# Optimization experiments

Hardware: AMD Instinct MI355X
Metric: run time of the kernel (lower is better)

Reference implementation:

```python
import jax, jax.numpy as jnp
import numpy as np

NUM_ROUTING = 3

def squash(v, axis=-1):
    # scale = s2 / (1 + s2) / sqrt(s2), same as the TF source (no epsilon)
    s2 = jnp.sum(jnp.square(v), axis=axis, keepdims=True)
    scale = s2 / (1.0 + s2) / jnp.sqrt(s2)
    return scale * v


def setup_inputs() -> dict:
    key = jax.random.key(0)
    k1, k2 = jax.random.split(key)
    B, I, D = 128, 1152, 8   # batch, input_num_capsule, input_dim_vector
    C, E = 32, 16            # num_capsule, dim_vector
    x = jax.random.normal(k1, (B, I, D), dtype=jnp.float32)
    W = jax.random.normal(k2, (I, C, D, E), dtype=jnp.float32) * 0.05
    return {"x": x, "W": W}


def reference(x, W):
    # x: [B, I, D]; W: [I, C, D, E]
    B, I, D = x.shape
    C, E = W.shape[1], W.shape[3]
    # inputs_hat: u_hat[b,i,c,e] = sum_d x[b,i,d] * W[i,c,d,e]
    # (the TF code serializes this over batch via tf.scan; math is a batched GEMM)
    u_hat = jnp.einsum('bid,icde->bice', x, W)  # [B, I, C, E]
    # routing logits; TF bias has shape [1, I, C, 1, 1] and becomes per-batch
    # [B, I, C, 1, 1] after the first += (broadcast). We track [*, I, C].
    b = jnp.zeros((1, I, C), dtype=x.dtype)
    outputs = None
    for i in range(NUM_ROUTING):
        c = jax.nn.softmax(b, axis=2)[..., None]           # [*, I, C, 1]
        s = jnp.sum(c * u_hat, axis=1, keepdims=True)      # [B, 1, C, E]
        outputs = squash(s)                                # [B, 1, C, E]
        if i != NUM_ROUTING - 1:
            b = b + jnp.sum(u_hat * outputs, axis=-1)      # [B, I, C]
    return outputs.reshape(B, C, E)
```

## Files before the change

kernel.cpp:

```cpp
#include <hip/hip_runtime.h>
#include <hip/hip_fp16.h>
#include <math.h>

#define BATCH 128
#define NI    1152
#define ND    8
#define NC    32
#define NE    16
#define NROUT 3

#define ISPLIT     128
#define ICHUNK     (NI / ISPLIT)
#define BT         16
#define NB         4
#define RT_THREADS 256
#define CROW       68
#define TLDSW      (NC * CROW)
#define TILEF      (NC * ND * NE)
#define SQ_THREADS 256

typedef _Float16 h2 __attribute__((ext_vector_type(2)));
typedef unsigned int uint;

__device__ __forceinline__ h2 cvt_pk(float a, float b) {
    auto r = __builtin_amdgcn_cvt_pkrtz(a, b);
    union { decltype(r) i; h2 o; } u; u.i = r; return u.o;
}
__device__ __forceinline__ uint h2u(h2 v) { union { h2 h; uint u; } x; x.h = v; return x.u; }
__device__ __forceinline__ h2 u2h(uint v) { union { uint u; h2 h; } x; x.u = v; return x.h; }

#if __has_builtin(__builtin_amdgcn_fdot2)
#define FDOT2(a, b, c) __builtin_amdgcn_fdot2((a), (b), (c), false)
#else
__device__ __forceinline__ float FDOT2(h2 a, h2 b, float c) {
    return c + (float)a.x * (float)b.x + (float)a.y * (float)b.y;
}
#endif

template<int CTRL>
__device__ __forceinline__ float dpp_add(float v) {
    int t = __builtin_amdgcn_update_dpp(0, __float_as_int(v), CTRL, 0xF, 0xF, true);
    return v + __int_as_float(t);
}

__device__ __forceinline__ float xor32_sum(float v) {
#if __has_builtin(__builtin_amdgcn_permlane32_swap)
    auto r = __builtin_amdgcn_permlane32_swap(__float_as_int(v), __float_as_int(v), false, false);
    return __int_as_float(r[0]) + __int_as_float(r[1]);
#else
    return v + __shfl_xor(v, 32);
#endif
}
__device__ __forceinline__ float xor16_sum(float v) {
#if __has_builtin(__builtin_amdgcn_permlane16_swap)
    auto r = __builtin_amdgcn_permlane16_swap(__float_as_int(v), __float_as_int(v), false, false);
    return __int_as_float(r[0]) + __int_as_float(r[1]);
#else
    int s = __builtin_amdgcn_ds_swizzle(__float_as_int(v), 0x401F);
    return v + __int_as_float(s);
#endif
}

__device__ __forceinline__ float sum_over_e8(float v) {
    v = dpp_add<0xB1>(v);
    v = dpp_add<0x4E>(v);
    v = dpp_add<0x141>(v);
    return v;
}

__global__ __launch_bounds__(RT_THREADS)
void route_iter_kernel(const float* __restrict__ x, const float* __restrict__ W,
                       const float* __restrict__ o_sum, void* __restrict__ s_part,
                       int iter, int nslice, int use_atomic)
{
    __shared__ uint Wh[ICHUNK * TLDSW];

    const int tid = threadIdx.x;
    const int c   = tid & 31;
    const int eh  = (tid >> 5) & 1;
    int wid;
    asm("v_mov_b32 %0, %1" : "=v"(wid) : "v"(tid >> 6));
    const int ic  = blockIdx.x;
    const int bt  = blockIdx.y;
    const int i0  = ic * ICHUNK;
    const int b0  = bt * BT + wid * NB;
    const int e0  = eh * 8;

    {
        const float4* wsrc = (const float4*)(W + (size_t)i0 * TILEF);
        const int p0 = tid;
#pragma unroll
        for (int t = 0; t < ICHUNK; ++t) {
            float4 fa[2], fb[2];
#pragma unroll
            for (int r = 0; r < 2; ++r) {
                int p  = p0 + r * RT_THREADS;
                int cc = p >> 4, q = p & 15;
                int dp = q >> 2, e4 = q & 3;
                int base = t * 1024 + cc * 32 + dp * 8 + e4;
                fa[r] = wsrc[base];
                fb[r] = wsrc[base + 4];
            }
#pragma unroll
            for (int r = 0; r < 2; ++r) {
                int p  = p0 + r * RT_THREADS;
                int cc = p >> 4, q = p & 15;
                int dp = q >> 2, e4 = q & 3;
                uint* wb = &Wh[t * TLDSW + cc * CROW + e4 * 16 + dp];
                wb[0]  = h2u(cvt_pk(fa[r].x, fb[r].x));
                wb[4]  = h2u(cvt_pk(fa[r].y, fb[r].y));
                wb[8]  = h2u(cvt_pk(fa[r].z, fb[r].z));
                wb[12] = h2u(cvt_pk(fa[r].w, fb[r].w));
            }
        }
    }

    float o_reg[NB][8];
    if (iter > 0) {
#pragma unroll
        for (int j = 0; j < NB; ++j) {
            const float4* op = (const float4*)(o_sum + ((size_t)(b0 + j) * NC + c) * NE + e0);
            float4 a = op[0], b = op[1];
            o_reg[j][0] = a.x; o_reg[j][1] = a.y; o_reg[j][2] = a.z; o_reg[j][3] = a.w;
            o_reg[j][4] = b.x; o_reg[j][5] = b.y; o_reg[j][6] = b.z; o_reg[j][7] = b.w;
        }
    }

    float s_acc[NB][8];
#pragma unroll
    for (int j = 0; j < NB; ++j)
#pragma unroll
        for (int e = 0; e < 8; ++e) s_acc[j][e] = 0.f;

    const float* xp[NB];
    float4 xnA[NB][2], xnB[NB][2];
#pragma unroll
    for (int j = 0; j < NB; ++j) {
        xp[j] = x + ((size_t)(b0 + j) * NI + i0) * ND;
        xnA[j][0] = *(const float4*)xp[j];
        xnA[j][1] = *(const float4*)(xp[j] + 4);
    }

    __syncthreads();

    const uint* wbase = &Wh[c * CROW + e0 * 4];

    auto body = [&](const float4 (&XC)[NB][2], float4 (&XN)[NB][2], int II) {
        if (II + 1 < ICHUNK) {
#pragma unroll
            for (int j = 0; j < NB; ++j) {
                xp[j] += ND;
                XN[j][0] = *(const float4*)xp[j];
                XN[j][1] = *(const float4*)(xp[j] + 4);
            }
        }

        h2 xq[NB][4];
#pragma unroll
        for (int j = 0; j < NB; ++j) {
            xq[j][0] = cvt_pk(XC[j][0].x, XC[j][0].y);
            xq[j][1] = cvt_pk(XC[j][0].z, XC[j][0].w);
            xq[j][2] = cvt_pk(XC[j][1].x, XC[j][1].y);
            xq[j][3] = cvt_pk(XC[j][1].z, XC[j][1].w);
        }

        const uint* wr = wbase + II * TLDSW;
        float uh[NB][8];
#pragma unroll
        for (int j = 0; j < NB; ++j)
#pragma unroll
            for (int e = 0; e < 8; ++e) uh[j][e] = 0.f;

#pragma unroll
        for (int er = 0; er < 8; ++er) {
            uint4 wv = *(const uint4*)(wr + er * 4);
            h2 w0 = u2h(wv.x), w1 = u2h(wv.y), w2 = u2h(wv.z), w3 = u2h(wv.w);
#pragma unroll
            for (int j = 0; j < NB; ++j) {
                float acc = uh[j][er];
                acc = FDOT2(xq[j][0], w0, acc);
                acc = FDOT2(xq[j][1], w1, acc);
                acc = FDOT2(xq[j][2], w2, acc);
                acc = FDOT2(xq[j][3], w3, acc);
                uh[j][er] = acc;
            }
        }

        if (iter > 0) {
#pragma unroll
            for (int j = 0; j < NB; ++j) {
                float lp = 0.f;
#pragma unroll
                for (int e = 0; e < 8; ++e) lp = fmaf(uh[j][e], o_reg[j][e], lp);
                lp = xor32_sum(lp);
                float el = __expf(lp);
                float v = dpp_add<0x140>(dpp_add<0x141>(
                          dpp_add<0x4E>(dpp_add<0xB1>(el))));
                float den = xor16_sum(v);
                float wgt = el * __builtin_amdgcn_rcpf(den);
#pragma unroll
                for (int e = 0; e < 8; ++e) s_acc[j][e] = fmaf(wgt, uh[j][e], s_acc[j][e]);
            }
        } else {
            const float wgt = 1.f / 32.f;
#pragma unroll
            for (int j = 0; j < NB; ++j)
#pragma unroll
                for (int e = 0; e < 8; ++e) s_acc[j][e] = fmaf(wgt, uh[j][e], s_acc[j][e]);
        }
    };

    body(xnA, xnB, 0);
    body(xnB, xnA, 1);
    body(xnA, xnB, 2);
    body(xnB, xnA, 3);
    body(xnA, xnB, 4);
    body(xnB, xnA, 5);
    body(xnA, xnB, 6);
    body(xnB, xnA, 7);
    body(xnA, xnB, 8);

    if (!use_atomic) {
        __half* sp = (__half*)s_part;
#pragma unroll
        for (int j = 0; j < NB; ++j) {
            __half* base = sp + (((size_t)ic * BATCH + (b0 + j)) * NC + c) * NE + e0;
            union { __half2 h2v[4]; uint4 u; } pk;
#pragma unroll
            for (int q = 0; q < 4; ++q)
                pk.h2v[q] = __floats2half2_rn(s_acc[j][2*q], s_acc[j][2*q+1]);
            *(uint4*)base = pk.u;
        }
    } else {
        float* sp = (float*)s_part;
        const int slice = ic & (nslice - 1);
#pragma unroll
        for (int j = 0; j < NB; ++j) {
            float* base = sp + (((size_t)slice * BATCH + (b0 + j)) * NC + c) * NE + e0;
#pragma unroll
            for (int e = 0; e < 8; ++e) atomicAdd(base + e, s_acc[j][e]);
        }
    }
}

__global__ __launch_bounds__(SQ_THREADS)
void squash_kernel(void* __restrict__ s_part, float* __restrict__ o_sum,
                   float* __restrict__ out, int iter, int nslice, int use_atomic)
{
    const int base2 = (blockIdx.x * SQ_THREADS + threadIdx.x) * 2;

    float a0 = 0.f, a1 = 0.f;
    if (!use_atomic) {
        const __half* sp = (const __half*)s_part;
#pragma unroll 8
        for (int k = 0; k < nslice; ++k) {
            __half2 v = *(const __half2*)(sp + (size_t)k * (BATCH * NC * NE) + base2);
            a0 += __low2float(v);
            a1 += __high2float(v);
        }
    } else {
        float* sp = (float*)s_part;
        for (int k = 0; k < nslice; ++k) {
            float2 v = *(float2*)(sp + (size_t)k * (BATCH * NC * NE) + base2);
            a0 += v.x; a1 += v.y;
            *(float2*)(sp + (size_t)k * (BATCH * NC * NE) + base2) = make_float2(0.f, 0.f);
        }
    }

    float q = sum_over_e8(a0 * a0 + a1 * a1);
    float scale = sqrtf(q) / (1.f + q);
    float o0 = scale * a0, o1 = scale * a1;

    if (iter == NROUT - 1) {
        *(float2*)(out + base2) = make_float2(o0, o1);
    } else if (iter == 0) {
        *(float2*)(o_sum + base2) = make_float2(o0, o1);
    } else {
        float2 prev = *(float2*)(o_sum + base2);
        *(float2*)(o_sum + base2) = make_float2(prev.x + o0, prev.y + o1);
    }
}

extern "C" void kernel_launch(void* const* d_in, const int* in_sizes, int n_in,
                              void* d_out, int out_size, void* d_ws, size_t ws_size,
                              hipStream_t stream) {
    const float* x = (const float*)d_in[0];
    const float* W = (const float*)d_in[1];
    float* out = (float*)d_out;

    const size_t slice_elems = (size_t)BATCH * NC * NE;

    float* o_sum  = (float*)d_ws;
    void*  s_part = (void*)(o_sum + slice_elems);

    int nslice, use_atomic;
    if (ws_size >= slice_elems * sizeof(float) + (size_t)ISPLIT * slice_elems * sizeof(__half)) {
        nslice = ISPLIT; use_atomic = 0;
    } else if (ws_size >= slice_elems * sizeof(float) * (32 + 1)) {
        nslice = 32; use_atomic = 1;
    } else {
        nslice = 8; use_atomic = 1;
    }

    if (use_atomic)
        (void)hipMemsetAsync(s_part, 0, slice_elems * sizeof(float) * nslice, stream);

    for (int it = 0; it < NROUT; ++it) {
        route_iter_kernel<<<dim3(ISPLIT, BATCH / BT), RT_THREADS, 0, stream>>>(
            x, W, o_sum, s_part, it, nslice, use_atomic);
        squash_kernel<<<(BATCH * NC * NE) / (SQ_THREADS * 2), SQ_THREADS, 0, stream>>>(
            s_part, o_sum, out, it, nslice, use_atomic);
    }
}
```

Baseline: 107.9 us.

## Pre-convert W to packed fp16 once and stream it from global in route kernel

```diff
diff --git a/kernel.cpp b/kernel.cpp
--- a/kernel.cpp
+++ b/kernel.cpp
@@ -9,15 +9,13 @@
 #define NE    16
 #define NROUT 3
 
-#define ISPLIT     128
+#define ISPLIT     48
 #define ICHUNK     (NI / ISPLIT)
 #define BT         16
 #define NB         4
 #define RT_THREADS 256
-#define CROW       68
-#define TLDSW      (NC * CROW)
-#define TILEF      (NC * ND * NE)
 #define SQ_THREADS 256
+#define PREP_TPB   2
 
 typedef _Float16 h2 __attribute__((ext_vector_type(2)));
 typedef unsigned int uint;
@@ -69,12 +67,48 @@
 }
 
 __global__ __launch_bounds__(RT_THREADS)
-void route_iter_kernel(const float* __restrict__ x, const float* __restrict__ W,
-                       const float* __restrict__ o_sum, void* __restrict__ s_part,
-                       int iter, int nslice, int use_atomic)
+void prep_kernel(const float* __restrict__ W, uint4* __restrict__ W_h)
 {
-    __shared__ uint Wh[ICHUNK * TLDSW];
-
+    __shared__ float ls[PREP_TPB][NC * 132];
+
+    const int tid = threadIdx.x;
+    const size_t i0 = (size_t)blockIdx.x * PREP_TPB;
+
+    const float4* src = (const float4*)(W + i0 * (NC * ND * NE));
+#pragma unroll
+    for (int t = 0; t < PREP_TPB; ++t) {
+#pragma unroll
+        for (int r = 0; r < 4; ++r) {
+            int g = tid + r * RT_THREADS;
+            float4 v = src[t * 1024 + g];
+            *(float4*)&ls[t][(g >> 5) * 132 + (g & 31) * 4] = v;
+        }
+    }
+    __syncthreads();
+
+#pragma unroll
+    for (int t = 0; t < PREP_TPB; ++t) {
+#pragma unroll
+        for (int r = 0; r < 2; ++r) {
+            int g  = tid + r * RT_THREADS;
+            int er = g >> 6, ehh = (g >> 5) & 1, c = g & 31;
+            int e  = ehh * 8 + er;
+            const float* p = &ls[t][c * 132 + e];
+            uint4 o;
+            o.x = h2u(cvt_pk(p[0],  p[16]));
+            o.y = h2u(cvt_pk(p[32], p[48]));
+            o.z = h2u(cvt_pk(p[64], p[80]));
+            o.w = h2u(cvt_pk(p[96], p[112]));
+            W_h[(i0 + t) * 512 + g] = o;
+        }
+    }
+}
+
+__global__ __launch_bounds__(RT_THREADS)
+void route_iter_kernel(const float* __restrict__ x, const uint4* __restrict__ W_h,
+                       const float* __restrict__ o_sum, __half* __restrict__ s_part,
+                       int iter)
+{
     const int tid = threadIdx.x;
     const int c   = tid & 31;
     const int eh  = (tid >> 5) & 1;
@@ -86,35 +120,6 @@
     const int b0  = bt * BT + wid * NB;
     const int e0  = eh * 8;
 
-    {
-        const float4* wsrc = (const float4*)(W + (size_t)i0 * TILEF);
-        const int p0 = tid;
-#pragma unroll
-        for (int t = 0; t < ICHUNK; ++t) {
-            float4 fa[2], fb[2];
-#pragma unroll
-            for (int r = 0; r < 2; ++r) {
-                int p  = p0 + r * RT_THREADS;
-                int cc = p >> 4, q = p & 15;
-                int dp = q >> 2, e4 = q & 3;
-                int base = t * 1024 + cc * 32 + dp * 8 + e4;
-                fa[r] = wsrc[base];
-                fb[r] = wsrc[base + 4];
-            }
-#pragma unroll
-            for (int r = 0; r < 2; ++r) {
-                int p  = p0 + r * RT_THREADS;
-                int cc = p >> 4, q = p & 15;
-                int dp = q >> 2, e4 = q & 3;
-                uint* wb = &Wh[t * TLDSW + cc * CROW + e4 * 16 + dp];
-                wb[0]  = h2u(cvt_pk(fa[r].x, fb[r].x));
-                wb[4]  = h2u(cvt_pk(fa[r].y, fb[r].y));
-                wb[8]  = h2u(cvt_pk(fa[r].z, fb[r].z));
-                wb[12] = h2u(cvt_pk(fa[r].w, fb[r].w));
-            }
-        }
-    }
-
     float o_reg[NB][8];
     if (iter > 0) {
 #pragma unroll
@@ -141,11 +146,14 @@
         xnA[j][1] = *(const float4*)(xp[j] + 4);
     }
 
-    __syncthreads();
-
-    const uint* wbase = &Wh[c * CROW + e0 * 4];
+    const uint4* wp = W_h + (size_t)i0 * 512 + eh * 32 + c;
 
     auto body = [&](const float4 (&XC)[NB][2], float4 (&XN)[NB][2], int II) {
+        uint4 wv[8];
+#pragma unroll
+        for (int er = 0; er < 8; ++er) wv[er] = wp[er * 64];
+        wp += 512;
+
         if (II + 1 < ICHUNK) {
 #pragma unroll
             for (int j = 0; j < NB; ++j) {
@@ -164,20 +172,14 @@
             xq[j][3] = cvt_pk(XC[j][1].z, XC[j][1].w);
         }
 
-        const uint* wr = wbase + II * TLDSW;
         float uh[NB][8];
 #pragma unroll
-        for (int j = 0; j < NB; ++j)
-#pragma unroll
-            for (int e = 0; e < 8; ++e) uh[j][e] = 0.f;
-
-#pragma unroll
         for (int er = 0; er < 8; ++er) {
-            uint4 wv = *(const uint4*)(wr + er * 4);
-            h2 w0 = u2h(wv.x), w1 = u2h(wv.y), w2 = u2h(wv.z), w3 = u2h(wv.w);
+            h2 w0 = u2h(wv[er].x), w1 = u2h(wv[er].y);
+            h2 w2 = u2h(wv[er].z), w3 = u2h(wv[er].w);
 #pragma unroll
             for (int j = 0; j < NB; ++j) {
-                float acc = uh[j][er];
+                float acc = 0.f;
                 acc = FDOT2(xq[j][0], w0, acc);
                 acc = FDOT2(xq[j][1], w1, acc);
                 acc = FDOT2(xq[j][2], w2, acc);
@@ -210,61 +212,34 @@
         }
     };
 
-    body(xnA, xnB, 0);
-    body(xnB, xnA, 1);
-    body(xnA, xnB, 2);
-    body(xnB, xnA, 3);
-    body(xnA, xnB, 4);
-    body(xnB, xnA, 5);
-    body(xnA, xnB, 6);
-    body(xnB, xnA, 7);
-    body(xnA, xnB, 8);
-
-    if (!use_atomic) {
-        __half* sp = (__half*)s_part;
-#pragma unroll
-        for (int j = 0; j < NB; ++j) {
-            __half* base = sp + (((size_t)ic * BATCH + (b0 + j)) * NC + c) * NE + e0;
-            union { __half2 h2v[4]; uint4 u; } pk;
-#pragma unroll
-            for (int q = 0; q < 4; ++q)
-                pk.h2v[q] = __floats2half2_rn(s_acc[j][2*q], s_acc[j][2*q+1]);
-            *(uint4*)base = pk.u;
-        }
-    } else {
-        float* sp = (float*)s_part;
-        const int slice = ic & (nslice - 1);
-#pragma unroll
-        for (int j = 0; j < NB; ++j) {
-            float* base = sp + (((size_t)slice * BATCH + (b0 + j)) * NC + c) * NE + e0;
-#pragma unroll
-            for (int e = 0; e < 8; ++e) atomicAdd(base + e, s_acc[j][e]);
-        }
+    for (int r2 = 0; r2 < ICHUNK / 2; ++r2) {
+        body(xnA, xnB, 2 * r2);
+        body(xnB, xnA, 2 * r2 + 1);
+    }
+
+#pragma unroll
+    for (int j = 0; j < NB; ++j) {
+        __half* base = s_part + (((size_t)ic * BATCH + (b0 + j)) * NC + c) * NE + e0;
+        union { __half2 h2v[4]; uint4 u; } pk;
+#pragma unroll
+        for (int q = 0; q < 4; ++q)
+            pk.h2v[q] = __floats2half2_rn(s_acc[j][2*q], s_acc[j][2*q+1]);
+        *(uint4*)base = pk.u;
     }
 }
 
 __global__ __launch_bounds__(SQ_THREADS)
-void squash_kernel(void* __restrict__ s_part, float* __restrict__ o_sum,
-                   float* __restrict__ out, int iter, int nslice, int use_atomic)
+void squash_kernel(const __half* __restrict__ s_part, float* __restrict__ o_sum,
+                   float* __restrict__ out, int iter)
 {
     const int base2 = (blockIdx.x * SQ_THREADS + threadIdx.x) * 2;
 
     float a0 = 0.f, a1 = 0.f;
-    if (!use_atomic) {
-        const __half* sp = (const __half*)s_part;
 #pragma unroll 8
-        for (int k = 0; k < nslice; ++k) {
-            __half2 v = *(const __half2*)(sp + (size_t)k * (BATCH * NC * NE) + base2);
-            a0 += __low2float(v);
-            a1 += __high2float(v);
-        }
-    } else {
-        float* sp = (float*)s_part;
-        for (int k = 0; k < nslice; ++k) {
-            float2 v = *(float2*)(sp + (size_t)k * (BATCH * NC * NE) + base2);
-            a0 += v.x; a1 += v.y;
-            *(float2*)(sp + (size_t)k * (BATCH * NC * NE) + base2) = make_float2(0.f, 0.f);
-        }
+    for (int k = 0; k < ISPLIT; ++k) {
+        __half2 v = *(const __half2*)(s_part + (size_t)k * (BATCH * NC * NE) + base2);
+        a0 += __low2float(v);
+        a1 += __high2float(v);
     }
 
     float q = sum_over_e8(a0 * a0 + a1 * a1);
@@ -288,27 +263,16 @@
     const float* W = (const float*)d_in[1];
     float* out = (float*)d_out;
 
-    const size_t slice_elems = (size_t)BATCH * NC * NE;
-
-    float* o_sum  = (float*)d_ws;
-    void*  s_part = (void*)(o_sum + slice_elems);
-
-    int nslice, use_atomic;
-    if (ws_size >= slice_elems * sizeof(float) + (size_t)ISPLIT * slice_elems * sizeof(__half)) {
-        nslice = ISPLIT; use_atomic = 0;
-    } else if (ws_size >= slice_elems * sizeof(float) * (32 + 1)) {
-        nslice = 32; use_atomic = 1;
-    } else {
-        nslice = 8; use_atomic = 1;
-    }
-
-    if (use_atomic)
-        (void)hipMemsetAsync(s_part, 0, slice_elems * sizeof(float) * nslice, stream);
+    uint4*  W_h    = (uint4*)d_ws;
+    __half* s_part = (__half*)(W_h + (size_t)NI * 512);
+    float*  o_sum  = (float*)(s_part + (size_t)ISPLIT * BATCH * NC * NE);
+
+    prep_kernel<<<NI / PREP_TPB, RT_THREADS, 0, stream>>>(W, W_h);
 
     for (int it = 0; it < NROUT; ++it) {
         route_iter_kernel<<<dim3(ISPLIT, BATCH / BT), RT_THREADS, 0, stream>>>(
-            x, W, o_sum, s_part, it, nslice, use_atomic);
+            x, W_h, o_sum, s_part, it);
         squash_kernel<<<(BATCH * NC * NE) / (SQ_THREADS * 2), SQ_THREADS, 0, stream>>>(
-            s_part, o_sum, out, it, nslice, use_atomic);
-    }
-}
+            s_part, o_sum, out, it);
+    }
+}
```

Result: slower. 124.8 us (+15.6%).
